# Kernel optimization log

Measured on AMD Instinct MI355X. Metric: run time of the kernel, lower is better.

The kernel has to match this reference:

```python
import jax, jax.numpy as jnp
import numpy as np

KH, KW, PAD, DIL, STRIDE = 3, 3, 1, 1, 1


def _conv2d(x, w):
    # plain dense conv, NCHW / OIHW, stride 1, pad 1
    return jax.lax.conv_general_dilated(
        x, w, window_strides=(STRIDE, STRIDE),
        padding=[(PAD, PAD), (PAD, PAD)],
        rhs_dilation=(DIL, DIL),
        dimension_numbers=('NCHW', 'OIHW', 'NCHW'))


def _deform_patches(x, offset):
    """Bilinear-sample deformable patches.
    x: [B,C,H,W], offset: [B,2K,Ho,Wo] with per-tap (dy,dx).
    Returns [B,C,K,Ho,Wo]."""
    B, C, H, W = x.shape
    Ho, Wo = offset.shape[2], offset.shape[3]
    K = KH * KW
    off = offset.reshape(B, K, 2, Ho, Wo)

    ky = jnp.repeat(jnp.arange(KH), KW)            # [K]
    kx = jnp.tile(jnp.arange(KW), KH)              # [K]
    base_y = (jnp.arange(Ho) * STRIDE - PAD)[None, :, None] + (DIL * ky)[:, None, None]  # [K,Ho,1]
    base_x = (jnp.arange(Wo) * STRIDE - PAD)[None, None, :] + (DIL * kx)[:, None, None]  # [K,1,Wo]

    sy = base_y[None].astype(x.dtype) + off[:, :, 0]   # [B,K,Ho,Wo]
    sx = base_x[None].astype(x.dtype) + off[:, :, 1]

    y0 = jnp.floor(sy); x0 = jnp.floor(sx)
    ly = sy - y0;       lx = sx - x0
    y0i = y0.astype(jnp.int32); x0i = x0.astype(jnp.int32)

    x_flat = x.reshape(B, C, H * W)

    def corner(yi, xi, wgt):
        valid = (yi >= 0) & (yi < H) & (xi >= 0) & (xi < W)   # zero padding outside
        idx = (jnp.clip(yi, 0, H - 1) * W + jnp.clip(xi, 0, W - 1))  # [B,K,Ho,Wo]
        gath = jax.vmap(lambda img, i: img[:, i.reshape(-1)])(x_flat, idx)  # [B,C,K*Ho*Wo]
        gath = gath.reshape(B, C, K, Ho, Wo)
        return gath * (wgt * valid.astype(x.dtype))[:, None]

    p = corner(y0i,     x0i,     (1 - ly) * (1 - lx))
    p = p + corner(y0i,     x0i + 1, (1 - ly) * lx)
    p = p + corner(y0i + 1, x0i,     ly * (1 - lx))
    p = p + corner(y0i + 1, x0i + 1, ly * lx)
    return p  # [B,C,K,Ho,Wo]


def setup_inputs() -> dict:
    key = jax.random.key(0)
    k1, k2, k3 = jax.random.split(key, 3)
    B, C, H, W = 8, 256, 64, 64
    Cout = 256
    x = jax.random.normal(k1, (B, C, H, W), dtype=jnp.float32)
    offset_w = jax.random.normal(k2, (2 * KH * KW, C, KH, KW), dtype=jnp.float32) * 0.02
    deform_w = jax.random.normal(k3, (Cout, C, KH, KW), dtype=jnp.float32) * 0.02
    return {"x": x, "offset_w": offset_w, "deform_w": deform_w}


def reference(x, offset_w, deform_w):
    # 1) offset-predicting conv
    offset = _conv2d(x, offset_w)                    # [B,2K,H,W]
    # 2) deformable conv = bilinear gather + contraction over (Cin, K)
    patches = _deform_patches(x, offset)             # [B,C,K,H,W]
    Cout = deform_w.shape[0]
    wk = deform_w.reshape(Cout, deform_w.shape[1], KH * KW)
    y = jnp.einsum('bckhw,ock->bohw', patches, wk)   # [B,Cout,H,W]
    # 3) avg + std channel attention (torch.std default: unbiased, ddof=1)
    avg = jnp.mean(y, axis=(2, 3), keepdims=True)
    std = jnp.std(y, axis=(2, 3), keepdims=True, ddof=1)
    attn = jax.nn.sigmoid(avg + std)
    return y * attn
```

## Files before the change

kernel.cpp:

```cpp
#include <hip/hip_runtime.h>
#include <hip/hip_bf16.h>
#include <math.h>

#define C_IN 256
#define H_   64
#define W_   64
#define B_   8
#define COUT 256
#define HW   (H_*W_)

typedef float f32x4 __attribute__((ext_vector_type(4)));
typedef float f32x2 __attribute__((ext_vector_type(2)));
typedef short short8 __attribute__((ext_vector_type(8)));

static __device__ __forceinline__ int pack_bf16x2(float a, float b) {
    __hip_bfloat162 h = __float22bfloat162_rn(make_float2(a, b));
    union { __hip_bfloat162 h; int i; } u; u.h = h;
    return u.i;
}

static __device__ __forceinline__ f32x2 up2(int v) {
    union { int i; float f; } a, b;
    a.i = v << 16;
    b.i = v & 0xffff0000;
    f32x2 r; r[0] = a.f; r[1] = b.f;
    return r;
}

static __device__ __forceinline__ void wg_barrier_lds() {
    asm volatile("s_waitcnt lgkmcnt(0)" ::: "memory");
    __builtin_amdgcn_s_barrier();
    __builtin_amdgcn_sched_barrier(0);
}

__global__ __launch_bounds__(256) void prep_weights_kernel(
    const float* __restrict__ ow, const float* __restrict__ dw,
    short* __restrict__ wR, short* __restrict__ wO)
{
    int blk = blockIdx.x;
    int k   = blk / 288;
    int row = blk % 288;
    int c   = threadIdx.x;
    int cblk = c >> 6, ks = (c >> 5) & 1, q = (c >> 3) & 3, ce = c & 7;
    union { float f; unsigned u; } a;
    if (row < 256) {
        int o = row;
        a.f = dw[(size_t)o * 2304 + c * 9 + k];
        unsigned r = (a.u + 0x7fffu + ((a.u >> 16) & 1u)) >> 16;
        size_t idx = (size_t)(k * 8 + cblk * 2 + ks) * 8192
                   + (size_t)(o >> 4) * 512 + q * 128 + (o & 15) * 8 + ce;
        wR[idx] = (short)r;
    } else {
        int o = row - 256;
        a.f = (o < 18) ? ow[(size_t)o * 2304 + c * 9 + k] : 0.f;
        unsigned r = (a.u + 0x7fffu + ((a.u >> 16) & 1u)) >> 16;
        size_t idx = (size_t)(k * 8 + cblk * 2 + ks) * 1024
                   + (size_t)(o >> 4) * 512 + q * 128 + (o & 15) * 8 + ce;
        wO[idx] = (short)r;
    }
}

__global__ __launch_bounds__(256) void transpose_x_kernel(
    const float* __restrict__ x, unsigned short* __restrict__ xT)
{
    __shared__ float tile[64][257];
    const int tid = threadIdx.x;
    const int b = blockIdx.x >> 6, h = blockIdx.x & 63;
    const float* xb = x + ((size_t)b << 20) + h * 64;

#pragma unroll
    for (int pass = 0; pass < 16; ++pass) {
        int c  = pass * 16 + (tid >> 4);
        int w0 = (tid & 15) * 4;
        float4 v = *(const float4*)(xb + (size_t)c * 4096 + w0);
        tile[w0][c] = v.x; tile[w0 + 1][c] = v.y;
        tile[w0 + 2][c] = v.z; tile[w0 + 3][c] = v.w;
    }
    __syncthreads();

    int4* ob = (int4*)(xT + ((size_t)blockIdx.x << 14));
#pragma unroll
    for (int pass = 0; pass < 8; ++pass) {
        int idx = pass * 256 + tid;
        int w = idx >> 5, ch8 = idx & 31;
        const float* tr = &tile[w][ch8 * 8];
        int4 pk;
        pk.x = pack_bf16x2(tr[0], tr[1]);
        pk.y = pack_bf16x2(tr[2], tr[3]);
        pk.z = pack_bf16x2(tr[4], tr[5]);
        pk.w = pack_bf16x2(tr[6], tr[7]);
        ob[idx] = pk;
    }
}

__global__ __launch_bounds__(256, 2) void offset_mfma_kernel(
    const unsigned short* __restrict__ xT, const short* __restrict__ wO,
    float* __restrict__ offs)
{
    __shared__ int4 bT[2][64 * 8];

    const int tid = threadIdx.x;
    const int b   = blockIdx.x & 7;
    const int ho  = blockIdx.x >> 3;

    const int px = tid >> 2;
    const int cg = tid & 3;
    const int wv = tid >> 6;
    const int ln = tid & 63;
    const int lo = ln & 15;
    const int quad = ln >> 4;
    const int pxl = wv * 16 + lo;

    f32x4 acc[2];
    acc[0] = (f32x4){0.f, 0.f, 0.f, 0.f};
    acc[1] = (f32x4){0.f, 0.f, 0.f, 0.f};

    const unsigned short* xbb = xT + ((size_t)b << 20);
    const int4 zero4 = {0, 0, 0, 0};

    auto stageB = [&](int s, int buf) {
        int k = s >> 2, c0 = (s & 3) << 6;
        int yy = ho + k / 3 - 1;
        int xx = px + k % 3 - 1;
        bool valid = (yy >= 0) & (yy < 64) & (xx >= 0) & (xx < 64);
        int yc = min(max(yy, 0), 63), xc = min(max(xx, 0), 63);
        const int4* src = (const int4*)(xbb + (((size_t)yc * 64 + xc) << 8) + c0 + cg * 16);
        int4 p0 = valid ? src[0] : zero4;
        int4 p1 = valid ? src[1] : zero4;
        bT[buf][px * 8 + ((2 * cg)     ^ (px & 7))] = p0;
        bT[buf][px * 8 + ((2 * cg + 1) ^ (px & 7))] = p1;
    };

    stageB(0, 0);
    __syncthreads();

    for (int s = 0; s < 36; ++s) {
        const int cur = s & 1;
        if (s < 35) stageB(s + 1, cur ^ 1);

        const int k = s >> 2;
        const short* wkb = wO + (size_t)(k * 8 + (s & 3) * 2) * 1024 + ln * 8;
#pragma unroll
        for (int ks = 0; ks < 2; ++ks) {
            int ch = ks * 4 + quad;
            short8 bfr = *(const short8*)&bT[cur][pxl * 8 + (ch ^ (pxl & 7))];
#pragma unroll
            for (int t = 0; t < 2; ++t) {
                short8 afr = *(const short8*)(wkb + ks * 1024 + t * 512);
                acc[t] = __builtin_amdgcn_mfma_f32_16x16x32_bf16(afr, bfr, acc[t], 0, 0, 0);
            }
        }
        __syncthreads();
    }

#pragma unroll
    for (int t = 0; t < 2; ++t) {
#pragma unroll
        for (int r = 0; r < 4; ++r) {
            int o = t * 16 + quad * 4 + r;
            if (o < 18)
                offs[((size_t)b * 18 + o) * HW + ho * 64 + wv * 16 + lo] = acc[t][r];
        }
    }
}

struct afrag { short8 v[2][4]; };

__global__ __launch_bounds__(256, 2) void deform_mfma_kernel(
    const unsigned short* __restrict__ xT, const float* __restrict__ offs,
    const short* __restrict__ wR, float* __restrict__ y,
    float* __restrict__ sum_, float* __restrict__ sumsq_)
{
    __shared__ int4   meta_i[576];
    __shared__ float4 meta_w[576];
    __shared__ int4   bT[2][64 * 8];

    const int tid = threadIdx.x;
    const int b   = blockIdx.x & 7;
    const int ho  = blockIdx.x >> 3;

    for (int e = tid; e < 576; e += 256) {
        int kk  = e >> 6;
        int pxe = e & 63;
        float dy = offs[((size_t)b * 18 + 2 * kk)     * HW + ho * W_ + pxe];
        float dx = offs[((size_t)b * 18 + 2 * kk + 1) * HW + ho * W_ + pxe];
        float sy = (float)(ho - 1 + kk / 3) + dy;
        float sx = (float)(pxe - 1 + kk % 3) + dx;
        float y0f = floorf(sy), x0f = floorf(sx);
        float ly = sy - y0f, lx = sx - x0f;
        int y0 = (int)y0f, x0 = (int)x0f;
        int y1 = y0 + 1, x1 = x0 + 1;
        float wy0 = 1.f - ly, wx0 = 1.f - lx;
        bool vy0 = (y0 >= 0) & (y0 < H_), vy1 = (y1 >= 0) & (y1 < H_);
        bool vx0 = (x0 >= 0) & (x0 < W_), vx1 = (x1 >= 0) & (x1 < W_);
        int cy0 = min(max(y0, 0), H_ - 1), cy1 = min(max(y1, 0), H_ - 1);
        int cx0 = min(max(x0, 0), W_ - 1), cx1 = min(max(x1, 0), W_ - 1);
        int4 ii; float4 ww;
        ii.x = (cy0 * W_ + cx0) << 9;  ww.x = wy0 * wx0 * ((vy0 & vx0) ? 1.f : 0.f);
        ii.y = (cy0 * W_ + cx1) << 9;  ww.y = wy0 * lx  * ((vy0 & vx1) ? 1.f : 0.f);
        ii.z = (cy1 * W_ + cx0) << 9;  ww.z = ly  * wx0 * ((vy1 & vx0) ? 1.f : 0.f);
        ii.w = (cy1 * W_ + cx1) << 9;  ww.w = ly  * lx  * ((vy1 & vx1) ? 1.f : 0.f);
        meta_i[e] = ii;
        meta_w[e] = ww;
    }

    const int px = tid >> 2;
    const int cg = tid & 3;
    const int wv = tid >> 6;
    const int ln = tid & 63;
    const int lo = ln & 15;
    const int quad = ln >> 4;

    f32x4 acc[4][4];
#pragma unroll
    for (int t = 0; t < 4; ++t)
#pragma unroll
        for (int p = 0; p < 4; ++p)
            acc[t][p] = (f32x4){0.f, 0.f, 0.f, 0.f};

    const char* xbb = (const char*)(xT + ((size_t)b << 20) + cg * 16);

#define ISSUE_G(S, G0,G1,G2,G3,G4,G5,G6,G7)                                   \
    {                                                                         \
        int kn_ = (S) >> 2, cn_ = ((S) & 3) << 7;                             \
        int4 ii_ = meta_i[kn_ * 64 + px];                                     \
        const char* xc_ = xbb + cn_;                                          \
        const int4* pA_ = (const int4*)(xc_ + ii_.x);                         \
        const int4* pB_ = (const int4*)(xc_ + ii_.y);                         \
        const int4* pC_ = (const int4*)(xc_ + ii_.z);                         \
        const int4* pD_ = (const int4*)(xc_ + ii_.w);                         \
        G0 = pA_[0]; G1 = pA_[1];                                             \
        G2 = pB_[0]; G3 = pB_[1];                                             \
        G4 = pC_[0]; G5 = pC_[1];                                             \
        G6 = pD_[0]; G7 = pD_[1];                                             \
    }

#define ISSUE_A(S, AF)                                                        \
    {                                                                         \
        const short* wkb_ = wR + (size_t)((((S) >> 2) * 8 + ((S) & 3) * 2))   \
                          * 8192 + wv * 2048 + ln * 8;                        \
        _Pragma("unroll")                                                     \
        for (int ks_ = 0; ks_ < 2; ++ks_)                                     \
            _Pragma("unroll")                                                 \
            for (int t_ = 0; t_ < 4; ++t_)                                    \
                AF.v[ks_][t_] = *(const short8*)(wkb_ + ks_ * 8192 + t_ * 512);\
    }

#define BLEND_W(S, BUF, G0,G1,G2,G3,G4,G5,G6,G7)                              \
    {                                                                         \
        int kn_ = (S) >> 2;                                                   \
        float4 w4_ = meta_w[kn_ * 64 + px];                                   \
        auto bl_ = [&](int av, int bv, int cv, int dv) -> int {               \
            f32x2 r_ = up2(av) * w4_.x + up2(bv) * w4_.y                      \
                     + up2(cv) * w4_.z + up2(dv) * w4_.w;                     \
            return pack_bf16x2(r_[0], r_[1]);                                 \
        };                                                                    \
        int4 o0_, o1_;                                                        \
        o0_.x = bl_(G0.x, G2.x, G4.x, G6.x);                                  \
        o0_.y = bl_(G0.y, G2.y, G4.y, G6.y);                                  \
        o0_.z = bl_(G0.z, G2.z, G4.z, G6.z);                                  \
        o0_.w = bl_(G0.w, G2.w, G4.w, G6.w);                                  \
        o1_.x = bl_(G1.x, G3.x, G5.x, G7.x);                                  \
        o1_.y = bl_(G1.y, G3.y, G5.y, G7.y);                                  \
        o1_.z = bl_(G1.z, G3.z, G5.z, G7.z);                                  \
        o1_.w = bl_(G1.w, G3.w, G5.w, G7.w);                                  \
        bT[BUF][px * 8 + ((2 * cg)     ^ (px & 7))] = o0_;                    \
        bT[BUF][px * 8 + ((2 * cg + 1) ^ (px & 7))] = o1_;                    \
    }

    auto mfmaStage = [&](int buf, const afrag& AF) {
        __builtin_amdgcn_s_setprio(1);
#pragma unroll
        for (int ks = 0; ks < 2; ++ks) {
            int ch = ks * 4 + quad;
            short8 bfr[4];
#pragma unroll
            for (int p = 0; p < 4; ++p) {
                int pp = p * 16 + lo;
                bfr[p] = *(const short8*)&bT[buf][pp * 8 + (ch ^ (pp & 7))];
            }
#pragma unroll
            for (int t = 0; t < 4; ++t)
#pragma unroll
                for (int p = 0; p < 4; ++p)
                    acc[t][p] = __builtin_amdgcn_mfma_f32_16x16x32_bf16(
                        AF.v[ks][t], bfr[p], acc[t][p], 0, 0, 0);
        }
        __builtin_amdgcn_s_setprio(0);
    };

    int4 a0, a1, a2, a3, a4, a5, a6, a7;
    int4 b0, b1, b2, b3, b4, b5, b6, b7;
    afrag afrA, afrB;

    wg_barrier_lds();

    ISSUE_A(0, afrA);
    ISSUE_G(0, a0,a1,a2,a3,a4,a5,a6,a7);
    ISSUE_G(1, b0,b1,b2,b3,b4,b5,b6,b7);
    BLEND_W(0, 0, a0,a1,a2,a3,a4,a5,a6,a7);
    wg_barrier_lds();

#pragma unroll 1
    for (int t = 0; t < 17; ++t) {
        int s = 2 * t;
        ISSUE_A(s + 1, afrB);
        ISSUE_G(s + 2, a0,a1,a2,a3,a4,a5,a6,a7);
        __builtin_amdgcn_sched_barrier(0);
        mfmaStage(0, afrA);
        BLEND_W(s + 1, 1, b0,b1,b2,b3,b4,b5,b6,b7);
        wg_barrier_lds();
        ISSUE_A(s + 2, afrA);
        ISSUE_G(s + 3, b0,b1,b2,b3,b4,b5,b6,b7);
        __builtin_amdgcn_sched_barrier(0);
        mfmaStage(1, afrB);
        BLEND_W(s + 2, 0, a0,a1,a2,a3,a4,a5,a6,a7);
        wg_barrier_lds();
    }
    ISSUE_A(35, afrB);
    __builtin_amdgcn_sched_barrier(0);
    mfmaStage(0, afrA);
    BLEND_W(35, 1, b0,b1,b2,b3,b4,b5,b6,b7);
    wg_barrier_lds();
    mfmaStage(1, afrB);

#undef ISSUE_G
#undef ISSUE_A
#undef BLEND_W

    float* yb = y + ((size_t)b << 20) + ho * 64;
#pragma unroll
    for (int t = 0; t < 4; ++t) {
#pragma unroll
        for (int r = 0; r < 4; ++r) {
            int o = wv * 64 + t * 16 + quad * 4 + r;
            float sv = 0.f, qv = 0.f;
#pragma unroll
            for (int p = 0; p < 4; ++p) {
                float val = acc[t][p][r];
                yb[(size_t)o * HW + p * 16 + lo] = val;
                sv += val;
                qv += val * val;
            }
#pragma unroll
            for (int m = 1; m <= 8; m <<= 1) {
                sv += __shfl_xor(sv, m, 16);
                qv += __shfl_xor(qv, m, 16);
            }
            if (lo == 0) {
                atomicAdd(&sum_[b * COUT + o], sv);
                atomicAdd(&sumsq_[b * COUT + o], qv);
            }
        }
    }
}

__global__ __launch_bounds__(256) void attn_scale_kernel(
    const float* __restrict__ sum_, const float* __restrict__ sumsq_,
    float* __restrict__ y)
{
    int bo = blockIdx.x;
    float s = sum_[bo], q = sumsq_[bo];
    float mean = s * (1.f / 4096.f);
    float var  = (q - s * s * (1.f / 4096.f)) * (1.f / 4095.f);
    float sd   = sqrtf(fmaxf(var, 0.f));
    float attn = 1.f / (1.f + expf(-(mean + sd)));
    float4* yp = (float4*)(y + (size_t)bo * HW);
#pragma unroll
    for (int i = 0; i < 4; ++i) {
        float4 v = yp[threadIdx.x + i * 256];
        v.x *= attn; v.y *= attn; v.z *= attn; v.w *= attn;
        yp[threadIdx.x + i * 256] = v;
    }
}

extern "C" void kernel_launch(void* const* d_in, const int* in_sizes, int n_in,
                              void* d_out, int out_size, void* d_ws, size_t ws_size,
                              hipStream_t stream)
{
    const float* x  = (const float*)d_in[0];
    const float* ow = (const float*)d_in[1];
    const float* dw = (const float*)d_in[2];
    float* out = (float*)d_out;
    float* ws  = (float*)d_ws;

    float*          offs = ws;
    unsigned short* xT   = (unsigned short*)(ws + 589824);
    short*          wR   = (short*)(xT + 8388608);
    short*          wO   = wR + 589824;
    float*          sum_ = (float*)(wO + 73728);
    float*          sumsq_ = sum_ + 2048;

    hipMemsetAsync(sum_, 0, 2 * 2048 * sizeof(float), stream);

    prep_weights_kernel<<<9 * 288, 256, 0, stream>>>(ow, dw, wR, wO);
    transpose_x_kernel<<<512, 256, 0, stream>>>(x, xT);
    offset_mfma_kernel<<<512, 256, 0, stream>>>(xT, wO, offs);
    deform_mfma_kernel<<<512, 256, 0, stream>>>(xT, offs, wR, out, sum_, sumsq_);
    attn_scale_kernel<<<2048, 256, 0, stream>>>(sum_, sumsq_, out);
}
```

Baseline: 187.2 us.

## Split deform kernel into half-row tiles to double grid and raise occupancy

Each deform block now handles 32 output pixels of one row instead of 64, so the grid doubles to 1024 blocks. Each thread gathers one 16-byte channel chunk per corner instead of two, and the accumulators shrink from 4x4 to 4x2 MFMA tiles. Launch bounds move to 3 blocks per CU. The intent is to raise parallelism and occupancy on a gather-latency-bound kernel, at the cost of loading each weight fragment twice as often per output pixel. The custom LDS barrier is replaced by __syncthreads.

```diff
diff --git a/kernel.cpp b/kernel.cpp
--- a/kernel.cpp
+++ b/kernel.cpp
@@ -25,12 +25,6 @@
     b.i = v & 0xffff0000;
     f32x2 r; r[0] = a.f; r[1] = b.f;
     return r;
-}
-
-static __device__ __forceinline__ void wg_barrier_lds() {
-    asm volatile("s_waitcnt lgkmcnt(0)" ::: "memory");
-    __builtin_amdgcn_s_barrier();
-    __builtin_amdgcn_sched_barrier(0);
 }
 
 __global__ __launch_bounds__(256) void prep_weights_kernel(
@@ -166,22 +160,24 @@
 
 struct afrag { short8 v[2][4]; };
 
-__global__ __launch_bounds__(256, 2) void deform_mfma_kernel(
+__global__ __launch_bounds__(256, 3) void deform_mfma_kernel(
     const unsigned short* __restrict__ xT, const float* __restrict__ offs,
     const short* __restrict__ wR, float* __restrict__ y,
     float* __restrict__ sum_, float* __restrict__ sumsq_)
 {
-    __shared__ int4   meta_i[576];
-    __shared__ float4 meta_w[576];
-    __shared__ int4   bT[2][64 * 8];
+    __shared__ int4   meta_i[288];
+    __shared__ float4 meta_w[288];
+    __shared__ int4   bT[2][32 * 8];
 
     const int tid = threadIdx.x;
     const int b   = blockIdx.x & 7;
-    const int ho  = blockIdx.x >> 3;
-
-    for (int e = tid; e < 576; e += 256) {
-        int kk  = e >> 6;
-        int pxe = e & 63;
+    const int ho  = (blockIdx.x >> 3) & 63;
+    const int xh  = blockIdx.x >> 9;
+    const int px0 = xh * 32;
+
+    for (int e = tid; e < 288; e += 256) {
+        int kk  = e >> 5;
+        int pxe = px0 + (e & 31);
         float dy = offs[((size_t)b * 18 + 2 * kk)     * HW + ho * W_ + pxe];
         float dx = offs[((size_t)b * 18 + 2 * kk + 1) * HW + ho * W_ + pxe];
         float sy = (float)(ho - 1 + kk / 3) + dy;
@@ -204,35 +200,31 @@
         meta_w[e] = ww;
     }
 
-    const int px = tid >> 2;
-    const int cg = tid & 3;
+    const int px = tid >> 3;
+    const int cg = tid & 7;
     const int wv = tid >> 6;
     const int ln = tid & 63;
     const int lo = ln & 15;
     const int quad = ln >> 4;
 
-    f32x4 acc[4][4];
+    f32x4 acc[4][2];
 #pragma unroll
     for (int t = 0; t < 4; ++t)
 #pragma unroll
-        for (int p = 0; p < 4; ++p)
+        for (int p = 0; p < 2; ++p)
             acc[t][p] = (f32x4){0.f, 0.f, 0.f, 0.f};
 
-    const char* xbb = (const char*)(xT + ((size_t)b << 20) + cg * 16);
-
-#define ISSUE_G(S, G0,G1,G2,G3,G4,G5,G6,G7)                                   \
+    const char* xbb = (const char*)xT + ((size_t)b << 21) + cg * 16;
+
+#define ISSUE_G(S, G0,G1,G2,G3)                                               \
     {                                                                         \
         int kn_ = (S) >> 2, cn_ = ((S) & 3) << 7;                             \
-        int4 ii_ = meta_i[kn_ * 64 + px];                                     \
+        int4 ii_ = meta_i[kn_ * 32 + px];                                     \
         const char* xc_ = xbb + cn_;                                          \
-        const int4* pA_ = (const int4*)(xc_ + ii_.x);                         \
-        const int4* pB_ = (const int4*)(xc_ + ii_.y);                         \
-        const int4* pC_ = (const int4*)(xc_ + ii_.z);                         \
-        const int4* pD_ = (const int4*)(xc_ + ii_.w);                         \
-        G0 = pA_[0]; G1 = pA_[1];                                             \
-        G2 = pB_[0]; G3 = pB_[1];                                             \
-        G4 = pC_[0]; G5 = pC_[1];                                             \
-        G6 = pD_[0]; G7 = pD_[1];                                             \
+        G0 = *(const int4*)(xc_ + ii_.x);                                     \
+        G1 = *(const int4*)(xc_ + ii_.y);                                     \
+        G2 = *(const int4*)(xc_ + ii_.z);                                     \
+        G3 = *(const int4*)(xc_ + ii_.w);                                     \
     }
 
 #define ISSUE_A(S, AF)                                                        \
@@ -246,26 +238,21 @@
                 AF.v[ks_][t_] = *(const short8*)(wkb_ + ks_ * 8192 + t_ * 512);\
     }
 
-#define BLEND_W(S, BUF, G0,G1,G2,G3,G4,G5,G6,G7)                              \
+#define BLEND_W(S, BUF, G0,G1,G2,G3)                                          \
     {                                                                         \
         int kn_ = (S) >> 2;                                                   \
-        float4 w4_ = meta_w[kn_ * 64 + px];                                   \
+        float4 w4_ = meta_w[kn_ * 32 + px];                                   \
         auto bl_ = [&](int av, int bv, int cv, int dv) -> int {               \
             f32x2 r_ = up2(av) * w4_.x + up2(bv) * w4_.y                      \
                      + up2(cv) * w4_.z + up2(dv) * w4_.w;                     \
             return pack_bf16x2(r_[0], r_[1]);                                 \
         };                                                                    \
-        int4 o0_, o1_;                                                        \
-        o0_.x = bl_(G0.x, G2.x, G4.x, G6.x);                                  \
-        o0_.y = bl_(G0.y, G2.y, G4.y, G6.y);                                  \
-        o0_.z = bl_(G0.z, G2.z, G4.z, G6.z);                                  \
-        o0_.w = bl_(G0.w, G2.w, G4.w, G6.w);                                  \
-        o1_.x = bl_(G1.x, G3.x, G5.x, G7.x);                                  \
-        o1_.y = bl_(G1.y, G3.y, G5.y, G7.y);                                  \
-        o1_.z = bl_(G1.z, G3.z, G5.z, G7.z);                                  \
-        o1_.w = bl_(G1.w, G3.w, G5.w, G7.w);                                  \
-        bT[BUF][px * 8 + ((2 * cg)     ^ (px & 7))] = o0_;                    \
-        bT[BUF][px * 8 + ((2 * cg + 1) ^ (px & 7))] = o1_;                    \
+        int4 o0_;                                                             \
+        o0_.x = bl_(G0.x, G1.x, G2.x, G3.x);                                  \
+        o0_.y = bl_(G0.y, G1.y, G2.y, G3.y);                                  \
+        o0_.z = bl_(G0.z, G1.z, G2.z, G3.z);                                  \
+        o0_.w = bl_(G0.w, G1.w, G2.w, G3.w);                                  \
+        bT[BUF][px * 8 + (cg ^ (px & 7))] = o0_;                              \
     }
 
     auto mfmaStage = [&](int buf, const afrag& AF) {
@@ -273,62 +260,62 @@
 #pragma unroll
         for (int ks = 0; ks < 2; ++ks) {
             int ch = ks * 4 + quad;
-            short8 bfr[4];
-#pragma unroll
-            for (int p = 0; p < 4; ++p) {
+            short8 bfr[2];
+#pragma unroll
+            for (int p = 0; p < 2; ++p) {
                 int pp = p * 16 + lo;
                 bfr[p] = *(const short8*)&bT[buf][pp * 8 + (ch ^ (pp & 7))];
             }
 #pragma unroll
             for (int t = 0; t < 4; ++t)
 #pragma unroll
-                for (int p = 0; p < 4; ++p)
+                for (int p = 0; p < 2; ++p)
                     acc[t][p] = __builtin_amdgcn_mfma_f32_16x16x32_bf16(
                         AF.v[ks][t], bfr[p], acc[t][p], 0, 0, 0);
         }
         __builtin_amdgcn_s_setprio(0);
     };
 
-    int4 a0, a1, a2, a3, a4, a5, a6, a7;
-    int4 b0, b1, b2, b3, b4, b5, b6, b7;
+    int4 a0, a1, a2, a3;
+    int4 b0, b1, b2, b3;
     afrag afrA, afrB;
 
-    wg_barrier_lds();
+    __syncthreads();
 
     ISSUE_A(0, afrA);
-    ISSUE_G(0, a0,a1,a2,a3,a4,a5,a6,a7);
-    ISSUE_G(1, b0,b1,b2,b3,b4,b5,b6,b7);
-    BLEND_W(0, 0, a0,a1,a2,a3,a4,a5,a6,a7);
-    wg_barrier_lds();
+    ISSUE_G(0, a0,a1,a2,a3);
+    ISSUE_G(1, b0,b1,b2,b3);
+    BLEND_W(0, 0, a0,a1,a2,a3);
+    __syncthreads();
 
 #pragma unroll 1
     for (int t = 0; t < 17; ++t) {
         int s = 2 * t;
         ISSUE_A(s + 1, afrB);
-        ISSUE_G(s + 2, a0,a1,a2,a3,a4,a5,a6,a7);
+        ISSUE_G(s + 2, a0,a1,a2,a3);
         __builtin_amdgcn_sched_barrier(0);
         mfmaStage(0, afrA);
-        BLEND_W(s + 1, 1, b0,b1,b2,b3,b4,b5,b6,b7);
-        wg_barrier_lds();
+        BLEND_W(s + 1, 1, b0,b1,b2,b3);
+        __syncthreads();
         ISSUE_A(s + 2, afrA);
-        ISSUE_G(s + 3, b0,b1,b2,b3,b4,b5,b6,b7);
+        ISSUE_G(s + 3, b0,b1,b2,b3);
         __builtin_amdgcn_sched_barrier(0);
         mfmaStage(1, afrB);
-        BLEND_W(s + 2, 0, a0,a1,a2,a3,a4,a5,a6,a7);
-        wg_barrier_lds();
+        BLEND_W(s + 2, 0, a0,a1,a2,a3);
+        __syncthreads();
     }
     ISSUE_A(35, afrB);
     __builtin_amdgcn_sched_barrier(0);
     mfmaStage(0, afrA);
-    BLEND_W(35, 1, b0,b1,b2,b3,b4,b5,b6,b7);
-    wg_barrier_lds();
+    BLEND_W(35, 1, b0,b1,b2,b3);
+    __syncthreads();
     mfmaStage(1, afrB);
 
 #undef ISSUE_G
 #undef ISSUE_A
 #undef BLEND_W
 
-    float* yb = y + ((size_t)b << 20) + ho * 64;
+    float* yb = y + ((size_t)b << 20) + ho * 64 + px0;
 #pragma unroll
     for (int t = 0; t < 4; ++t) {
 #pragma unroll
@@ -336,7 +323,7 @@
             int o = wv * 64 + t * 16 + quad * 4 + r;
             float sv = 0.f, qv = 0.f;
 #pragma unroll
-            for (int p = 0; p < 4; ++p) {
+            for (int p = 0; p < 2; ++p) {
                 float val = acc[t][p][r];
                 yb[(size_t)o * HW + p * 16 + lo] = val;
                 sv += val;
@@ -396,6 +383,6 @@
     prep_weights_kernel<<<9 * 288, 256, 0, stream>>>(ow, dw, wR, wO);
     transpose_x_kernel<<<512, 256, 0, stream>>>(x, xT);
     offset_mfma_kernel<<<512, 256, 0, stream>>>(xT, wO, offs);
-    deform_mfma_kernel<<<512, 256, 0, stream>>>(xT, offs, wR, out, sum_, sumsq_);
+    deform_mfma_kernel<<<1024, 256, 0, stream>>>(xT, offs, wR, out, sum_, sumsq_);
     attn_scale_kernel<<<2048, 256, 0, stream>>>(sum_, sumsq_, out);
 }
```

Result: slower. 199.9 us (+6.8%).

## Fuse attention scaling into deform kernel via grid barrier; restage offset conv per tap

Applied to the files above, without the earlier changes.

The deform kernel now keeps its output in registers, waits at a global atomic grid barrier until all blocks have accumulated channel sums, then applies the sigmoid(mean+std) scale and writes y once. This removes the separate attention kernel and its extra read and write of the full output. The offset conv is restructured to stage a whole tap's 256 channels in LDS per step, giving 9 stages instead of 36 with larger swizzled tiles. The grid barrier assumes all 512 blocks are co-resident (2 per CU), and its spin has a bounded iteration cap, so a timeout could yield wrong results.

```diff
diff --git a/kernel.cpp b/kernel.cpp
--- a/kernel.cpp
+++ b/kernel.cpp
@@ -8,6 +8,7 @@
 #define B_   8
 #define COUT 256
 #define HW   (H_*W_)
+#define NBLK_DEF 512
 
 typedef float f32x4 __attribute__((ext_vector_type(4)));
 typedef float f32x2 __attribute__((ext_vector_type(2)));
@@ -25,12 +26,6 @@
     b.i = v & 0xffff0000;
     f32x2 r; r[0] = a.f; r[1] = b.f;
     return r;
-}
-
-static __device__ __forceinline__ void wg_barrier_lds() {
-    asm volatile("s_waitcnt lgkmcnt(0)" ::: "memory");
-    __builtin_amdgcn_s_barrier();
-    __builtin_amdgcn_sched_barrier(0);
 }
 
 __global__ __launch_bounds__(256) void prep_weights_kernel(
@@ -97,14 +92,14 @@
     const unsigned short* __restrict__ xT, const short* __restrict__ wO,
     float* __restrict__ offs)
 {
-    __shared__ int4 bT[2][64 * 8];
+    __shared__ int4 bT[64 * 32];
 
     const int tid = threadIdx.x;
     const int b   = blockIdx.x & 7;
     const int ho  = blockIdx.x >> 3;
 
     const int px = tid >> 2;
-    const int cg = tid & 3;
+    const int cs = tid & 3;
     const int wv = tid >> 6;
     const int ln = tid & 63;
     const int lo = ln & 15;
@@ -118,40 +113,65 @@
     const unsigned short* xbb = xT + ((size_t)b << 20);
     const int4 zero4 = {0, 0, 0, 0};
 
-    auto stageB = [&](int s, int buf) {
-        int k = s >> 2, c0 = (s & 3) << 6;
-        int yy = ho + k / 3 - 1;
-        int xx = px + k % 3 - 1;
-        bool valid = (yy >= 0) & (yy < 64) & (xx >= 0) & (xx < 64);
-        int yc = min(max(yy, 0), 63), xc = min(max(xx, 0), 63);
-        const int4* src = (const int4*)(xbb + (((size_t)yc * 64 + xc) << 8) + c0 + cg * 16);
-        int4 p0 = valid ? src[0] : zero4;
-        int4 p1 = valid ? src[1] : zero4;
-        bT[buf][px * 8 + ((2 * cg)     ^ (px & 7))] = p0;
-        bT[buf][px * 8 + ((2 * cg + 1) ^ (px & 7))] = p1;
-    };
-
-    stageB(0, 0);
-    __syncthreads();
-
-    for (int s = 0; s < 36; ++s) {
-        const int cur = s & 1;
-        if (s < 35) stageB(s + 1, cur ^ 1);
-
-        const int k = s >> 2;
-        const short* wkb = wO + (size_t)(k * 8 + (s & 3) * 2) * 1024 + ln * 8;
-#pragma unroll
-        for (int ks = 0; ks < 2; ++ks) {
-            int ch = ks * 4 + quad;
-            short8 bfr = *(const short8*)&bT[cur][pxl * 8 + (ch ^ (pxl & 7))];
+#define OG_LOAD(K, G)                                                         \
+    {                                                                         \
+        int yy_ = ho + (K) / 3 - 1, xx_ = px + (K) % 3 - 1;                   \
+        int yc_ = min(max(yy_, 0), 63), xc_ = min(max(xx_, 0), 63);           \
+        const int4* sp_ = (const int4*)(xbb + (((size_t)(yc_ * 64 + xc_)) << 8)\
+                                        + cs * 64);                           \
+        _Pragma("unroll")                                                     \
+        for (int j = 0; j < 8; ++j) G[j] = sp_[j];                            \
+    }
+#define OG_COMMIT(K, G)                                                       \
+    {                                                                         \
+        int yy_ = ho + (K) / 3 - 1, xx_ = px + (K) % 3 - 1;                   \
+        bool v_ = (yy_ >= 0) & (yy_ < 64) & (xx_ >= 0) & (xx_ < 64);          \
+        _Pragma("unroll")                                                     \
+        for (int j = 0; j < 8; ++j) {                                         \
+            int sl_ = (cs * 8 + j) ^ (px & 31);                               \
+            bT[px * 32 + sl_] = v_ ? G[j] : zero4;                            \
+        }                                                                     \
+    }
+
+    auto mfmaK = [&](int k) {
+        __builtin_amdgcn_s_setprio(1);
+#pragma unroll
+        for (int ksg = 0; ksg < 8; ++ksg) {
+            int sl = (ksg * 4 + quad) ^ (pxl & 31);
+            short8 bfr = *(const short8*)&bT[pxl * 32 + sl];
+            const short* wkb = wO + (size_t)(k * 8 + ksg) * 1024 + ln * 8;
 #pragma unroll
             for (int t = 0; t < 2; ++t) {
-                short8 afr = *(const short8*)(wkb + ks * 1024 + t * 512);
+                short8 afr = *(const short8*)(wkb + t * 512);
                 acc[t] = __builtin_amdgcn_mfma_f32_16x16x32_bf16(afr, bfr, acc[t], 0, 0, 0);
             }
         }
-        __syncthreads();
-    }
+        __builtin_amdgcn_s_setprio(0);
+    };
+
+    int4 ga[8], gb[8];
+    OG_LOAD(0, ga);
+#pragma unroll
+    for (int t2 = 0; t2 < 4; ++t2) {
+        int k = 2 * t2;
+        OG_COMMIT(k, ga);
+        __syncthreads();
+        OG_LOAD(k + 1, gb);
+        __builtin_amdgcn_sched_barrier(0);
+        mfmaK(k);
+        __syncthreads();
+        OG_COMMIT(k + 1, gb);
+        __syncthreads();
+        OG_LOAD(k + 2, ga);
+        __builtin_amdgcn_sched_barrier(0);
+        mfmaK(k + 1);
+        __syncthreads();
+    }
+    OG_COMMIT(8, ga);
+    __syncthreads();
+    mfmaK(8);
+#undef OG_LOAD
+#undef OG_COMMIT
 
 #pragma unroll
     for (int t = 0; t < 2; ++t) {
@@ -159,7 +179,7 @@
         for (int r = 0; r < 4; ++r) {
             int o = t * 16 + quad * 4 + r;
             if (o < 18)
-                offs[((size_t)b * 18 + o) * HW + ho * 64 + wv * 16 + lo] = acc[t][r];
+                offs[((size_t)b * 18 + o) * HW + ho * 64 + pxl] = acc[t][r];
         }
     }
 }
@@ -169,7 +189,7 @@
 __global__ __launch_bounds__(256, 2) void deform_mfma_kernel(
     const unsigned short* __restrict__ xT, const float* __restrict__ offs,
     const short* __restrict__ wR, float* __restrict__ y,
-    float* __restrict__ sum_, float* __restrict__ sumsq_)
+    float* __restrict__ sum_, float* __restrict__ sumsq_, int* __restrict__ bar)
 {
     __shared__ int4   meta_i[576];
     __shared__ float4 meta_w[576];
@@ -293,13 +313,13 @@
     int4 b0, b1, b2, b3, b4, b5, b6, b7;
     afrag afrA, afrB;
 
-    wg_barrier_lds();
+    __syncthreads();
 
     ISSUE_A(0, afrA);
     ISSUE_G(0, a0,a1,a2,a3,a4,a5,a6,a7);
     ISSUE_G(1, b0,b1,b2,b3,b4,b5,b6,b7);
     BLEND_W(0, 0, a0,a1,a2,a3,a4,a5,a6,a7);
-    wg_barrier_lds();
+    __syncthreads();
 
 #pragma unroll 1
     for (int t = 0; t < 17; ++t) {
@@ -309,26 +329,25 @@
         __builtin_amdgcn_sched_barrier(0);
         mfmaStage(0, afrA);
         BLEND_W(s + 1, 1, b0,b1,b2,b3,b4,b5,b6,b7);
-        wg_barrier_lds();
+        __syncthreads();
         ISSUE_A(s + 2, afrA);
         ISSUE_G(s + 3, b0,b1,b2,b3,b4,b5,b6,b7);
         __builtin_amdgcn_sched_barrier(0);
         mfmaStage(1, afrB);
         BLEND_W(s + 2, 0, a0,a1,a2,a3,a4,a5,a6,a7);
-        wg_barrier_lds();
+        __syncthreads();
     }
     ISSUE_A(35, afrB);
     __builtin_amdgcn_sched_barrier(0);
     mfmaStage(0, afrA);
     BLEND_W(35, 1, b0,b1,b2,b3,b4,b5,b6,b7);
-    wg_barrier_lds();
+    __syncthreads();
     mfmaStage(1, afrB);
 
 #undef ISSUE_G
 #undef ISSUE_A
 #undef BLEND_W
 
-    float* yb = y + ((size_t)b << 20) + ho * 64;
 #pragma unroll
     for (int t = 0; t < 4; ++t) {
 #pragma unroll
@@ -338,7 +357,6 @@
 #pragma unroll
             for (int p = 0; p < 4; ++p) {
                 float val = acc[t][p][r];
-                yb[(size_t)o * HW + p * 16 + lo] = val;
                 sv += val;
                 qv += val * val;
             }
@@ -353,24 +371,36 @@
             }
         }
     }
-}
-
-__global__ __launch_bounds__(256) void attn_scale_kernel(
-    const float* __restrict__ sum_, const float* __restrict__ sumsq_,
-    float* __restrict__ y)
-{
-    int bo = blockIdx.x;
-    float s = sum_[bo], q = sumsq_[bo];
-    float mean = s * (1.f / 4096.f);
-    float var  = (q - s * s * (1.f / 4096.f)) * (1.f / 4095.f);
-    float sd   = sqrtf(fmaxf(var, 0.f));
-    float attn = 1.f / (1.f + expf(-(mean + sd)));
-    float4* yp = (float4*)(y + (size_t)bo * HW);
-#pragma unroll
-    for (int i = 0; i < 4; ++i) {
-        float4 v = yp[threadIdx.x + i * 256];
-        v.x *= attn; v.y *= attn; v.z *= attn; v.w *= attn;
-        yp[threadIdx.x + i * 256] = v;
+
+    __syncthreads();
+    __threadfence();
+    if (tid == 0) {
+        atomicAdd(bar, 1);
+        int it = 0;
+        while (__hip_atomic_load(bar, __ATOMIC_ACQUIRE,
+                                 __HIP_MEMORY_SCOPE_AGENT) < NBLK_DEF
+               && it < (1 << 22)) ++it;
+    }
+    __syncthreads();
+
+    float* yb = y + ((size_t)b << 20) + ho * 64;
+#pragma unroll
+    for (int t = 0; t < 4; ++t) {
+#pragma unroll
+        for (int r = 0; r < 4; ++r) {
+            int o = wv * 64 + t * 16 + quad * 4 + r;
+            float s = __hip_atomic_load(&sum_[b * COUT + o],
+                                        __ATOMIC_RELAXED, __HIP_MEMORY_SCOPE_AGENT);
+            float q = __hip_atomic_load(&sumsq_[b * COUT + o],
+                                        __ATOMIC_RELAXED, __HIP_MEMORY_SCOPE_AGENT);
+            float mean = s * (1.f / 4096.f);
+            float var  = (q - s * s * (1.f / 4096.f)) * (1.f / 4095.f);
+            float sd   = sqrtf(fmaxf(var, 0.f));
+            float attn = 1.f / (1.f + expf(-(mean + sd)));
+#pragma unroll
+            for (int p = 0; p < 4; ++p)
+                yb[(size_t)o * HW + p * 16 + lo] = acc[t][p][r] * attn;
+        }
     }
 }
 
@@ -390,12 +420,13 @@
     short*          wO   = wR + 589824;
     float*          sum_ = (float*)(wO + 73728);
     float*          sumsq_ = sum_ + 2048;
-
-    hipMemsetAsync(sum_, 0, 2 * 2048 * sizeof(float), stream);
+    int*            bar  = (int*)(sumsq_ + 2048);
+
+    hipMemsetAsync(sum_, 0, (2 * 2048 + 4) * sizeof(float), stream);
 
     prep_weights_kernel<<<9 * 288, 256, 0, stream>>>(ow, dw, wR, wO);
     transpose_x_kernel<<<512, 256, 0, stream>>>(x, xT);
     offset_mfma_kernel<<<512, 256, 0, stream>>>(xT, wO, offs);
-    deform_mfma_kernel<<<512, 256, 0, stream>>>(xT, offs, wR, out, sum_, sumsq_);
-    attn_scale_kernel<<<2048, 256, 0, stream>>>(sum_, sumsq_, out);
-}
+    deform_mfma_kernel<<<NBLK_DEF, 256, 0, stream>>>(xT, offs, wR, out,
+                                                     sum_, sumsq_, bar);
+}
```

Measured after the change: 284.8 us. +52.1%, slower.

## Stage 3-row halo tile in offset conv and reuse across all nine taps

Applied to the files above, without the earlier changes.

The offset-prediction kernel now loads a 3x66 halo tile of input rows per 64-channel chunk into LDS once and reuses it for all 9 kernel taps. Before, it re-gathered a 64-pixel slice for each of the 36 tap/chunk stages with a barrier every stage. This cuts global loads and barriers to 4 chunks, at the cost of larger LDS use and one idle wave during staging. Separately, the custom LDS barrier helper in the deform kernel is replaced by plain __syncthreads, which may change scheduling there.

```diff
diff --git a/kernel.cpp b/kernel.cpp
--- a/kernel.cpp
+++ b/kernel.cpp
@@ -25,12 +25,6 @@
     b.i = v & 0xffff0000;
     f32x2 r; r[0] = a.f; r[1] = b.f;
     return r;
-}
-
-static __device__ __forceinline__ void wg_barrier_lds() {
-    asm volatile("s_waitcnt lgkmcnt(0)" ::: "memory");
-    __builtin_amdgcn_s_barrier();
-    __builtin_amdgcn_sched_barrier(0);
 }
 
 __global__ __launch_bounds__(256) void prep_weights_kernel(
@@ -97,19 +91,16 @@
     const unsigned short* __restrict__ xT, const short* __restrict__ wO,
     float* __restrict__ offs)
 {
-    __shared__ int4 bT[2][64 * 8];
+    __shared__ int4 xtile[3 * 66 * 8];
 
     const int tid = threadIdx.x;
     const int b   = blockIdx.x & 7;
     const int ho  = blockIdx.x >> 3;
 
-    const int px = tid >> 2;
-    const int cg = tid & 3;
     const int wv = tid >> 6;
     const int ln = tid & 63;
     const int lo = ln & 15;
     const int quad = ln >> 4;
-    const int pxl = wv * 16 + lo;
 
     f32x4 acc[2];
     acc[0] = (f32x4){0.f, 0.f, 0.f, 0.f};
@@ -118,40 +109,89 @@
     const unsigned short* xbb = xT + ((size_t)b << 20);
     const int4 zero4 = {0, 0, 0, 0};
 
-    auto stageB = [&](int s, int buf) {
-        int k = s >> 2, c0 = (s & 3) << 6;
-        int yy = ho + k / 3 - 1;
-        int xx = px + k % 3 - 1;
-        bool valid = (yy >= 0) & (yy < 64) & (xx >= 0) & (xx < 64);
-        int yc = min(max(yy, 0), 63), xc = min(max(xx, 0), 63);
-        const int4* src = (const int4*)(xbb + (((size_t)yc * 64 + xc) << 8) + c0 + cg * 16);
-        int4 p0 = valid ? src[0] : zero4;
-        int4 p1 = valid ? src[1] : zero4;
-        bT[buf][px * 8 + ((2 * cg)     ^ (px & 7))] = p0;
-        bT[buf][px * 8 + ((2 * cg + 1) ^ (px & 7))] = p1;
-    };
-
-    stageB(0, 0);
-    __syncthreads();
-
-    for (int s = 0; s < 36; ++s) {
-        const int cur = s & 1;
-        if (s < 35) stageB(s + 1, cur ^ 1);
-
-        const int k = s >> 2;
-        const short* wkb = wO + (size_t)(k * 8 + (s & 3) * 2) * 1024 + ln * 8;
-#pragma unroll
-        for (int ks = 0; ks < 2; ++ks) {
-            int ch = ks * 4 + quad;
-            short8 bfr = *(const short8*)&bT[cur][pxl * 8 + (ch ^ (pxl & 7))];
-#pragma unroll
-            for (int t = 0; t < 2; ++t) {
-                short8 afr = *(const short8*)(wkb + ks * 1024 + t * 512);
-                acc[t] = __builtin_amdgcn_mfma_f32_16x16x32_bf16(afr, bfr, acc[t], 0, 0, 0);
+    const int srow = tid >> 6;
+    const int spx  = tid & 63;
+    const int syy  = ho + srow - 1;
+    const bool svalid = (srow < 3) && (syy >= 0) && (syy < 64);
+    const int syc  = min(max(syy, 0), 63);
+    const unsigned short* sbase = xbb + (((size_t)(syc * 64 + spx)) << 8);
+    const int sslot = spx + 1;
+
+#define OLOAD(CH, G)                                                          \
+    if (srow < 3) {                                                           \
+        const int4* sp_ = (const int4*)(sbase + (CH));                        \
+        _Pragma("unroll")                                                     \
+        for (int j = 0; j < 8; ++j) G[j] = sp_[j];                            \
+    }
+#define OCOMMIT(G)                                                            \
+    if (srow < 3) {                                                           \
+        _Pragma("unroll")                                                     \
+        for (int j = 0; j < 8; ++j)                                           \
+            xtile[(srow * 66 + sslot) * 8 + (j ^ (sslot & 7))]                \
+                = svalid ? G[j] : zero4;                                      \
+    }
+
+    auto mfmaC = [&](int chunk) {
+        __builtin_amdgcn_s_setprio(1);
+#pragma unroll
+        for (int ky = 0; ky < 3; ++ky) {
+#pragma unroll
+            for (int kx = 0; kx < 3; ++kx) {
+#pragma unroll
+                for (int ks = 0; ks < 2; ++ks) {
+                    int ps = wv * 16 + lo + kx;
+                    int cslot = (ks * 4 + quad) ^ (ps & 7);
+                    short8 bfr = *(const short8*)&xtile[(ky * 66 + ps) * 8 + cslot];
+                    const short* wkb = wO
+                        + (size_t)((ky * 3 + kx) * 8 + chunk * 2 + ks) * 1024
+                        + ln * 8;
+#pragma unroll
+                    for (int t = 0; t < 2; ++t) {
+                        short8 afr = *(const short8*)(wkb + t * 512);
+                        acc[t] = __builtin_amdgcn_mfma_f32_16x16x32_bf16(
+                            afr, bfr, acc[t], 0, 0, 0);
+                    }
+                }
             }
         }
-        __syncthreads();
-    }
+        __builtin_amdgcn_s_setprio(0);
+    };
+
+    int4 ga[8], gb[8];
+    OLOAD(0, ga);
+    OCOMMIT(ga);
+    if (srow == 3 && (tid & 63) < 6) {
+        int idx = tid & 63;
+        int row_ = idx >> 1, s_ = (idx & 1) * 65;
+#pragma unroll
+        for (int j = 0; j < 8; ++j) xtile[(row_ * 66 + s_) * 8 + j] = zero4;
+    }
+    __syncthreads();
+
+    OLOAD(64, gb);
+    __builtin_amdgcn_sched_barrier(0);
+    mfmaC(0);
+    __syncthreads();
+    OCOMMIT(gb);
+    __syncthreads();
+
+    OLOAD(128, ga);
+    __builtin_amdgcn_sched_barrier(0);
+    mfmaC(1);
+    __syncthreads();
+    OCOMMIT(ga);
+    __syncthreads();
+
+    OLOAD(192, gb);
+    __builtin_amdgcn_sched_barrier(0);
+    mfmaC(2);
+    __syncthreads();
+    OCOMMIT(gb);
+    __syncthreads();
+
+    mfmaC(3);
+#undef OLOAD
+#undef OCOMMIT
 
 #pragma unroll
     for (int t = 0; t < 2; ++t) {
@@ -293,13 +333,13 @@
     int4 b0, b1, b2, b3, b4, b5, b6, b7;
     afrag afrA, afrB;
 
-    wg_barrier_lds();
+    __syncthreads();
 
     ISSUE_A(0, afrA);
     ISSUE_G(0, a0,a1,a2,a3,a4,a5,a6,a7);
     ISSUE_G(1, b0,b1,b2,b3,b4,b5,b6,b7);
     BLEND_W(0, 0, a0,a1,a2,a3,a4,a5,a6,a7);
-    wg_barrier_lds();
+    __syncthreads();
 
 #pragma unroll 1
     for (int t = 0; t < 17; ++t) {
@@ -309,19 +349,19 @@
         __builtin_amdgcn_sched_barrier(0);
         mfmaStage(0, afrA);
         BLEND_W(s + 1, 1, b0,b1,b2,b3,b4,b5,b6,b7);
-        wg_barrier_lds();
+        __syncthreads();
         ISSUE_A(s + 2, afrA);
         ISSUE_G(s + 3, b0,b1,b2,b3,b4,b5,b6,b7);
         __builtin_amdgcn_sched_barrier(0);
         mfmaStage(1, afrB);
         BLEND_W(s + 2, 0, a0,a1,a2,a3,a4,a5,a6,a7);
-        wg_barrier_lds();
+        __syncthreads();
     }
     ISSUE_A(35, afrB);
     __builtin_amdgcn_sched_barrier(0);
     mfmaStage(0, afrA);
     BLEND_W(35, 1, b0,b1,b2,b3,b4,b5,b6,b7);
-    wg_barrier_lds();
+    __syncthreads();
     mfmaStage(1, afrB);
 
 #undef ISSUE_G
```

Measured after the change: 199.2 us, median of 2. +6.4%, slower.
